# Performance work log

Hardware: AMD Instinct MI355X
Metric: run time of the kernel (lower is better)

## Reference

```python
import jax, jax.numpy as jnp
import numpy as np

B, S, D, H, E, K = 2, 2048, 1024, 16, 8, 2
HD = D // H          # head dim = 64 (single shared KV head: MQA)
HID = 4 * D          # MoE expert hidden dim


def _rmsnorm(x):
    # zeta SimpleRMSNorm: F.normalize(x, dim=-1) * dim**0.5
    n = jnp.linalg.norm(x, axis=-1, keepdims=True)
    return x / jnp.maximum(n, 1e-12) * (D ** 0.5)


def setup_inputs() -> dict:
    key = jax.random.key(0)
    ks = jax.random.split(key, 8)
    def w(k, shape, fan_in):
        return jax.random.normal(k, shape, jnp.float32) * (fan_in ** -0.5)
    return {
        "x":  jax.random.normal(ks[0], (B, S, D), jnp.float32),
        "Wq": w(ks[1], (D, D), D),
        "Wk": w(ks[2], (D, HD), D),
        "Wv": w(ks[3], (D, HD), D),
        "Wo": w(ks[4], (D, D), D),
        "Wg": w(ks[5], (D, E), D),
        "W1": w(ks[6], (E, D, HID), D),
        "W2": w(ks[7], (E, HID, D), HID),
    }


def reference(x, Wq, Wk, Wv, Wo, Wg, W1, W2):
    skip = x
    # --- pre-norm + multi-query attention + residual ---
    h = _rmsnorm(x)
    q = (h @ Wq).reshape(B, S, H, HD)           # [B,S,H,HD]
    k = h @ Wk                                   # [B,S,HD] shared kv head
    v = h @ Wv                                   # [B,S,HD]
    scores = jnp.einsum('bqhd,bkd->bhqk', q, k) * (HD ** -0.5)
    attn = jax.nn.softmax(scores, axis=-1)
    o = jnp.einsum('bhqk,bkd->bqhd', attn, v).reshape(B, S, D) @ Wo
    x = o + h
    # --- pre-norm + MoE (top-k softmax gating over experts) ---
    h2 = _rmsnorm(x)
    logits = h2 @ Wg                             # [B,S,E]
    topv, topi = jax.lax.top_k(logits, K)        # [B,S,K]
    gate = jax.nn.softmax(topv, axis=-1)         # renormalized top-k weights
    # dense combine weights [B,S,E], zero for unselected experts
    dense_w = jnp.sum(jax.nn.one_hot(topi, E, dtype=h2.dtype) * gate[..., None], axis=-2)
    moe_out = jnp.zeros_like(h2)
    for e in range(E):  # fixed small expert count
        ffn = jax.nn.gelu(h2 @ W1[e]) @ W2[e]
        moe_out = moe_out + dense_w[..., e:e + 1] * ffn
    return moe_out + skip
```

## Files before the change

kernel.cpp:

```cpp
#include <hip/hip_runtime.h>

typedef __bf16 bf16x8 __attribute__((ext_vector_type(8)));
typedef float f32x4 __attribute__((ext_vector_type(4)));
using u16 = unsigned short;
using u32 = unsigned int;

#define B_   2
#define S_   2048
#define D_   1024
#define E_   8
#define HID_ 4096
#define M_   4096

__device__ __forceinline__ u16 f2b_rne(float f) {
    unsigned u = __float_as_uint(f);
    u += 0x7fffu + ((u >> 16) & 1u);
    return (u16)(u >> 16);
}
__device__ __forceinline__ float b2f(u16 h) { return __uint_as_float(((unsigned)h) << 16); }
__device__ __forceinline__ void split2(float v, u16& h, u16& m) {
    h = f2b_rne(v); m = f2b_rne(v - b2f(h));
}
__device__ __forceinline__ void gld16(void* l, const void* g) {
    __builtin_amdgcn_global_load_lds((const __attribute__((address_space(1))) u32*)g,
                                     (__attribute__((address_space(3))) u32*)l, 16, 0, 0);
}

static constexpr size_t OFF_WQKVT0 = 0;
static constexpr size_t OFF_WQKVT1 = OFF_WQKVT0 + (size_t)1152*1024*2;
static constexpr size_t OFF_WOT    = OFF_WQKVT1 + (size_t)1152*1024*2;
static constexpr size_t OFF_W1T    = OFF_WOT    + (size_t)1024*1024*2;
static constexpr size_t OFF_W2T    = OFF_W1T    + (size_t)E_*HID_*D_*2;
static constexpr size_t OFF_WOWG   = OFF_W2T    + (size_t)E_*HID_*D_*2;
static constexpr size_t OFF_HF32   = OFF_WOWG   + (size_t)1024*8*4;
static constexpr size_t OFF_H0     = OFF_HF32   + (size_t)M_*D_*4;
static constexpr size_t OFF_H1     = OFF_H0     + (size_t)M_*D_*2;
static constexpr size_t OFF_H2     = OFF_H1     + (size_t)M_*D_*2;
static constexpr size_t OFF_CTL    = OFF_H2     + (size_t)M_*D_*2;
static constexpr size_t OFF_TEXP   = OFF_CTL    + 512;
static constexpr size_t OFF_TGATE  = OFF_TEXP   + (size_t)M_*2*4;
static constexpr size_t OFF_R2T    = OFF_TGATE  + (size_t)M_*2*4;
static constexpr size_t OFF_T2R    = OFF_R2T    + (size_t)9216*4;
static constexpr size_t OFF_ZROW   = OFF_T2R    + (size_t)M_*2*4;
static constexpr size_t OFF_BIG    = OFF_ZROW   + 4096;
static constexpr size_t OFF_Q0     = OFF_BIG;
static constexpr size_t OFF_Q1     = OFF_Q0   + (size_t)M_*D_*2;
static constexpr size_t OFF_KF0    = OFF_Q1   + (size_t)M_*D_*2;
static constexpr size_t OFF_KF1    = OFF_KF0  + (size_t)2*128*2*512*2;
static constexpr size_t OFF_VF0    = OFF_KF1  + (size_t)2*128*2*512*2;
static constexpr size_t OFF_VF1    = OFF_VF0  + (size_t)2*64*4*512*2;
static constexpr size_t OFF_OF32   = OFF_VF1  + (size_t)2*64*4*512*2;
static constexpr size_t OFF_AOBF   = OFF_OF32 + (size_t)M_*D_*4;
static constexpr size_t OFF_XF32   = OFF_Q0;
static constexpr size_t OFF_TACT   = OFF_BIG;
static constexpr size_t OFF_CONTR  = OFF_TACT + (size_t)9216*HID_*2;

__global__ __launch_bounds__(256) void transpose_split2_k(const float* __restrict__ in,
        u16* __restrict__ o0, u16* __restrict__ o1, int R, int C)
{
    __shared__ float tile[32][33];
    int tx = threadIdx.x & 31, ty = threadIdx.x >> 5;
    int c0 = blockIdx.x * 32, r0 = blockIdx.y * 32;
#pragma unroll
    for (int k = 0; k < 4; ++k)
        tile[ty + k*8][tx] = in[(size_t)(r0 + ty + k*8)*C + c0 + tx];
    __syncthreads();
#pragma unroll
    for (int k = 0; k < 4; ++k) {
        float v = tile[tx][ty + k*8];
        u16 h, m; split2(v, h, m);
        size_t idx = (size_t)(c0 + ty + k*8)*R + r0 + tx;
        o0[idx] = h; o1[idx] = m;
    }
}

__global__ __launch_bounds__(256) void transpose_k(const float* __restrict__ in,
                                                   u16* __restrict__ out, int R, int C)
{
    __shared__ u16 tile[32][33];
    int bz = blockIdx.z;
    in  += (size_t)bz * R * C;
    out += (size_t)bz * R * C;
    int tx = threadIdx.x & 31, ty = threadIdx.x >> 5;
    int c0 = blockIdx.x * 32, r0 = blockIdx.y * 32;
#pragma unroll
    for (int k = 0; k < 4; ++k)
        tile[ty + k*8][tx] = f2b_rne(in[(size_t)(r0 + ty + k*8)*C + c0 + tx]);
    __syncthreads();
#pragma unroll
    for (int k = 0; k < 4; ++k)
        out[(size_t)(c0 + ty + k*8)*R + r0 + tx] = tile[tx][ty + k*8];
}

__global__ __launch_bounds__(64) void wowg_k(const float* __restrict__ Wo,
                                             const float* __restrict__ Wg,
                                             float* __restrict__ wowg)
{
    int i = blockIdx.x, lane = threadIdx.x;
    const float* wr = Wo + (size_t)i*1024;
    float acc[8] = {};
#pragma unroll
    for (int j = 0; j < 16; ++j) {
        int d = j*64 + lane;
        float wv = wr[d];
        const float* g = Wg + (size_t)d*8;
        float4 g0 = *(const float4*)g, g1 = *(const float4*)(g + 4);
        acc[0] += wv*g0.x; acc[1] += wv*g0.y; acc[2] += wv*g0.z; acc[3] += wv*g0.w;
        acc[4] += wv*g1.x; acc[5] += wv*g1.y; acc[6] += wv*g1.z; acc[7] += wv*g1.w;
    }
#pragma unroll
    for (int e = 0; e < 8; ++e)
#pragma unroll
        for (int o = 32; o; o >>= 1) acc[e] += __shfl_down(acc[e], o);
    if (lane == 0) {
#pragma unroll
        for (int e = 0; e < 8; ++e) wowg[i*8 + e] = acc[e];
    }
}

__global__ __launch_bounds__(256) void rmsnorm1_k(const float* __restrict__ x,
                                                  float* __restrict__ hf,
                                                  u16* __restrict__ h0, u16* __restrict__ h1)
{
    int row = blockIdx.x, t = threadIdx.x;
    float4 v = ((const float4*)(x + (size_t)row*1024))[t];
    float ss = v.x*v.x + v.y*v.y + v.z*v.z + v.w*v.w;
#pragma unroll
    for (int o = 32; o; o >>= 1) ss += __shfl_down(ss, o);
    __shared__ float red[4];
    if ((t & 63) == 0) red[t >> 6] = ss;
    __syncthreads();
    float tot = red[0] + red[1] + red[2] + red[3];
    float sc = 32.0f / fmaxf(sqrtf(tot), 1e-12f);
    float vv[4] = {v.x*sc, v.y*sc, v.z*sc, v.w*sc};
    ((float4*)(hf + (size_t)row*1024))[t] = *(float4*)vv;
    u16 a0[4], a1[4];
#pragma unroll
    for (int j = 0; j < 4; ++j) split2(vv[j], a0[j], a1[j]);
    *(uint2*)(h0 + (size_t)row*1024 + t*4) = *(uint2*)a0;
    *(uint2*)(h1 + (size_t)row*1024 + t*4) = *(uint2*)a1;
}

__device__ __forceinline__ void gemm_pass(const u16* __restrict__ gA0, const u16* __restrict__ gB0,
                                          u16* As, u16* Bs, f32x4 (&acc)[4][4],
                                          int t, const int (&aoff)[4], const int (&boff)[4])
{
    const u16* gA1 = gA0 + (size_t)64*1024;
    const u16* gB1 = gB0 + (size_t)64*1024;
    uint4 ra0 = *(const uint4*)gA0, ra1 = *(const uint4*)gA1;
    uint4 rb0 = *(const uint4*)gB0, rb1 = *(const uint4*)gB1;
    for (int kt = 0; kt < 32; ++kt) {
        __syncthreads();
        *(uint4*)((char*)As + t*16)        = ra0;
        *(uint4*)((char*)As + 4096 + t*16) = ra1;
        *(uint4*)((char*)Bs + t*16)        = rb0;
        *(uint4*)((char*)Bs + 4096 + t*16) = rb1;
        __syncthreads();
        if (kt + 1 < 32) {
            int k0 = (kt + 1)*32;
            ra0 = *(const uint4*)(gA0 + k0); ra1 = *(const uint4*)(gA1 + k0);
            rb0 = *(const uint4*)(gB0 + k0); rb1 = *(const uint4*)(gB1 + k0);
        }
        bf16x8 av[4], bv[4];
#pragma unroll
        for (int i = 0; i < 4; ++i) av[i] = *(const bf16x8*)((char*)As + aoff[i]);
#pragma unroll
        for (int i = 0; i < 4; ++i) bv[i] = *(const bf16x8*)((char*)Bs + boff[i]);
#pragma unroll
        for (int mi = 0; mi < 4; ++mi)
#pragma unroll
            for (int ni = 0; ni < 4; ++ni)
                acc[mi][ni] = __builtin_amdgcn_mfma_f32_16x16x32_bf16(av[mi], bv[ni], acc[mi][ni], 0, 0, 0);
    }
}

__global__ __launch_bounds__(256) void gemm_qkv(
    const u16* __restrict__ A0, const u16* __restrict__ A1,
    const u16* __restrict__ B0, const u16* __restrict__ B1,
    u16* __restrict__ q0, u16* __restrict__ q1,
    u16* __restrict__ kf0, u16* __restrict__ kf1,
    u16* __restrict__ vf0, u16* __restrict__ vf1)
{
    int rb = blockIdx.x, cb = blockIdx.y;
    __shared__ __attribute__((aligned(16))) u16 As[4096];
    __shared__ __attribute__((aligned(16))) u16 Bs[4096];
    int t = threadIdx.x, w = t >> 6, lane = t & 63, r = lane & 15, g = lane >> 4;
    int wr = w >> 1, wc = w & 1;
    int arow0 = t >> 2, colA = (t & 3)*8;
    int aoff[4], boff[4];
#pragma unroll
    for (int i = 0; i < 4; ++i) {
        aoff[i] = ((wr*64 + i*16 + r)*32 + g*8)*2;
        boff[i] = ((wc*64 + i*16 + r)*32 + g*8)*2;
    }
    f32x4 acc[4][4] = {};
    const u16* Aps[3]; const u16* Bps[3];
    Aps[0] = A0; Aps[1] = A0; Aps[2] = A1;
    Bps[0] = B0; Bps[1] = B1; Bps[2] = B0;
#pragma unroll
    for (int c = 0; c < 3; ++c) {
        const u16* Ab = Aps[c] + (size_t)(rb*128 + arow0)*1024 + colA;
        const u16* Bb = Bps[c] + (size_t)(cb*128 + arow0)*1024 + colA;
        gemm_pass(Ab, Bb, As, Bs, acc, t, aoff, boff);
    }
    int bm = rb*128, bn = cb*128;
#pragma unroll
    for (int mi = 0; mi < 4; ++mi)
#pragma unroll
        for (int ni = 0; ni < 4; ++ni) {
            int row0 = bm + wr*64 + mi*16 + g*4;
            int col  = bn + wc*64 + ni*16 + r;
#pragma unroll
            for (int reg = 0; reg < 4; ++reg) {
                float val = acc[mi][ni][reg];
                int rr = row0 + reg;
                if (col < 1024) {
                    u16 hh, mm; split2(val * 0.125f, hh, mm);
                    size_t idx = (size_t)rr*1024 + col;
                    q0[idx] = hh; q1[idx] = mm;
                } else {
                    int c = col - 1024;
                    u16 hh, mm; split2(val, hh, mm);
                    int bb = rr >> 11, kv = rr & 2047;
                    if (c < 64) {
                        int ntg = kv >> 4, r2 = kv & 15, kc = c >> 5, gg = (c >> 3) & 3, j = c & 7;
                        size_t off = ((((size_t)bb*128 + ntg)*2 + kc)*64 + gg*16 + r2)*8 + j;
                        kf0[off] = hh; kf1[off] = mm;
                    } else {
                        int d = c - 64;
                        int ntg = d >> 4, r2 = d & 15, kvc = kv >> 5, gg = (kv >> 3) & 3, j = kv & 7;
                        size_t off = ((((size_t)bb*64 + kvc)*4 + ntg)*64 + gg*16 + r2)*8 + j;
                        vf0[off] = hh; vf1[off] = mm;
                    }
                }
            }
        }
}

__global__ __launch_bounds__(256) void attn_k(
    const u16* __restrict__ q0, const u16* __restrict__ q1,
    const u16* __restrict__ kfr0, const u16* __restrict__ kfr1,
    const u16* __restrict__ vfr0, const u16* __restrict__ vfr1,
    float* __restrict__ of32, u16* __restrict__ obf)
{
    int qt = blockIdx.x, h = blockIdx.y, b = blockIdx.z;
    int t = threadIdx.x, w = t >> 6, lane = t & 63, r = lane & 15, g = lane >> 4;
    __shared__ __attribute__((aligned(16))) char smem[40960];
    char* plw = smem + 32768 + w*2048;

    const char* K0c = (const char*)kfr0;
    const char* K1c = (const char*)kfr1;
    const char* V0c = (const char*)vfr0;
    const char* V1c = (const char*)vfr1;

    int qrow = b*2048 + qt*64 + w*16 + r;
    bf16x8 qf0[2], qf1[2];
#pragma unroll
    for (int kc = 0; kc < 2; ++kc) {
        size_t qi = (size_t)qrow*1024 + h*64 + kc*32 + g*8;
        qf0[kc] = *(const bf16x8*)(q0 + qi);
        qf1[kc] = *(const bf16x8*)(q1 + qi);
    }

    f32x4 accO[4] = {};
    float mrun[4], lrun[4];
#pragma unroll
    for (int reg = 0; reg < 4; ++reg) { mrun[reg] = -1e30f; lrun[reg] = 0.f; }

    for (int kt = 0; kt < 32; ++kt) {
        __syncthreads();
        {
            size_t kb = ((size_t)(b*128 + kt*4))*2048;
            gld16(smem +         t*16, K0c + kb + t*16);
            gld16(smem + 4096  + t*16, K0c + kb + 4096 + t*16);
            gld16(smem + 8192  + t*16, K1c + kb + t*16);
            gld16(smem + 12288 + t*16, K1c + kb + 4096 + t*16);
            size_t vb = ((size_t)(b*64 + kt*2))*4096;
            gld16(smem + 16384 + t*16, V0c + vb + t*16);
            gld16(smem + 20480 + t*16, V0c + vb + 4096 + t*16);
            gld16(smem + 24576 + t*16, V1c + vb + t*16);
            gld16(smem + 28672 + t*16, V1c + vb + 4096 + t*16);
        }
        __syncthreads();

        f32x4 s[4] = {};
#pragma unroll
        for (int nt = 0; nt < 4; ++nt)
#pragma unroll
            for (int kc = 0; kc < 2; ++kc) {
                bf16x8 kf0 = *(const bf16x8*)(smem + (nt*2 + kc)*1024 + lane*16);
                bf16x8 kf1 = *(const bf16x8*)(smem + 8192 + (nt*2 + kc)*1024 + lane*16);
                s[nt] = __builtin_amdgcn_mfma_f32_16x16x32_bf16(qf0[kc], kf0, s[nt], 0, 0, 0);
                s[nt] = __builtin_amdgcn_mfma_f32_16x16x32_bf16(qf0[kc], kf1, s[nt], 0, 0, 0);
                s[nt] = __builtin_amdgcn_mfma_f32_16x16x32_bf16(qf1[kc], kf0, s[nt], 0, 0, 0);
            }

#pragma unroll
        for (int reg = 0; reg < 4; ++reg) {
            float mx = fmaxf(fmaxf(s[0][reg], s[1][reg]), fmaxf(s[2][reg], s[3][reg]));
#pragma unroll
            for (int d = 1; d < 16; d <<= 1) mx = fmaxf(mx, __shfl_xor(mx, d));
            float mn = fmaxf(mrun[reg], mx);
            float alpha = __expf(mrun[reg] - mn);
            float ls = 0.f;
#pragma unroll
            for (int nt = 0; nt < 4; ++nt) {
                float pv = __expf(s[nt][reg] - mn);
                s[nt][reg] = pv; ls += pv;
            }
#pragma unroll
            for (int d = 1; d < 16; d <<= 1) ls += __shfl_xor(ls, d);
            lrun[reg] = lrun[reg]*alpha + ls;
            mrun[reg] = mn;
#pragma unroll
            for (int nt = 0; nt < 4; ++nt) accO[nt][reg] *= alpha;
        }

#pragma unroll
        for (int ps = 0; ps < 2; ++ps) {
#pragma unroll
            for (int nt = 0; nt < 4; ++nt)
#pragma unroll
                for (int reg = 0; reg < 4; ++reg) {
                    float pv = s[nt][reg];
                    u16 hh = f2b_rne(pv);
                    if (ps) hh = f2b_rne(pv - b2f(hh));
                    int gr = g*4 + reg;
                    int off = (gr*128 + (nt*16 + r)*2) ^ ((gr & 7) << 4);
                    *(u16*)(plw + off) = hh;
                }
#pragma unroll
            for (int kc = 0; kc < 2; ++kc) {
                int po = (r*128 + kc*64 + g*16) ^ ((r & 7) << 4);
                bf16x8 pf = *(const bf16x8*)(plw + po);
#pragma unroll
                for (int nt = 0; nt < 4; ++nt) {
                    bf16x8 vf0 = *(const bf16x8*)(smem + 16384 + (kc*4 + nt)*1024 + lane*16);
                    accO[nt] = __builtin_amdgcn_mfma_f32_16x16x32_bf16(pf, vf0, accO[nt], 0, 0, 0);
                    if (ps == 0) {
                        bf16x8 vf1 = *(const bf16x8*)(smem + 24576 + (kc*4 + nt)*1024 + lane*16);
                        accO[nt] = __builtin_amdgcn_mfma_f32_16x16x32_bf16(pf, vf1, accO[nt], 0, 0, 0);
                    }
                }
            }
        }
    }

#pragma unroll
    for (int nt = 0; nt < 4; ++nt)
#pragma unroll
        for (int reg = 0; reg < 4; ++reg) {
            float o = accO[nt][reg] / lrun[reg];
            int row = b*2048 + qt*64 + w*16 + g*4 + reg;
            size_t idx = (size_t)row*1024 + h*64 + nt*16 + r;
            of32[idx] = o;
            obf[idx] = f2b_rne(o);
        }
}

template<int EP, bool MOE, bool INDIR>
__global__ __launch_bounds__(256) void gemm1(
    const u16* __restrict__ Abase, const u16* __restrict__ Bbase,
    u16* __restrict__ outb, float* __restrict__ outf, const float* __restrict__ addsrc,
    const int* __restrict__ r2t, const int* __restrict__ ctl, const u16* __restrict__ zrow,
    int K, int N)
{
    int rb = blockIdx.x, cb = blockIdx.y;
    if (MOE) { if (rb*128 >= ctl[16]) return; }
    const u16* Bt = Bbase;
    if (MOE) Bt += (size_t)ctl[32 + rb] * N * K;

    __shared__ __attribute__((aligned(16))) u16 As[4096];
    __shared__ __attribute__((aligned(16))) u16 Bs[4096];
    int t = threadIdx.x, w = t >> 6, lane = t & 63, r = lane & 15, g = lane >> 4;
    int wr = w >> 1, wc = w & 1;
    int arow0 = t >> 2, colA = (t & 3)*8;

    const char *gA0c, *gA1c;
    if (INDIR) {
        int tk0 = r2t[rb*128 + arow0];
        int tk1 = r2t[rb*128 + 64 + arow0];
        gA0c = (const char*)((tk0 < 0 ? zrow : Abase + (size_t)tk0*K) + colA);
        gA1c = (const char*)((tk1 < 0 ? zrow : Abase + (size_t)tk1*K) + colA);
    } else {
        gA0c = (const char*)(Abase + (size_t)(rb*128 + arow0)*K + colA);
        gA1c = (const char*)(Abase + (size_t)(rb*128 + 64 + arow0)*K + colA);
    }
    const char* gB0c = (const char*)(Bt + (size_t)(cb*128 + arow0)*K + colA);
    const char* gB1c = (const char*)(Bt + (size_t)(cb*128 + 64 + arow0)*K + colA);

    int aoff[4], boff[4];
#pragma unroll
    for (int i = 0; i < 4; ++i) {
        aoff[i] = ((wr*64 + i*16 + r)*32 + g*8)*2;
        boff[i] = ((wc*64 + i*16 + r)*32 + g*8)*2;
    }
    f32x4 acc[4][4] = {};
    int nk = K >> 5;
    for (int kt = 0; kt < nk; ++kt) {
        __syncthreads();
        gld16((char*)As + t*16,        gA0c + kt*64);
        gld16((char*)As + 4096 + t*16, gA1c + kt*64);
        gld16((char*)Bs + t*16,        gB0c + kt*64);
        gld16((char*)Bs + 4096 + t*16, gB1c + kt*64);
        __syncthreads();
        bf16x8 av[4], bv[4];
#pragma unroll
        for (int i = 0; i < 4; ++i) av[i] = *(const bf16x8*)((char*)As + aoff[i]);
#pragma unroll
        for (int i = 0; i < 4; ++i) bv[i] = *(const bf16x8*)((char*)Bs + boff[i]);
#pragma unroll
        for (int mi = 0; mi < 4; ++mi)
#pragma unroll
            for (int ni = 0; ni < 4; ++ni)
                acc[mi][ni] = __builtin_amdgcn_mfma_f32_16x16x32_bf16(av[mi], bv[ni], acc[mi][ni], 0, 0, 0);
    }

    int bm = rb*128, bn = cb*128;
#pragma unroll
    for (int mi = 0; mi < 4; ++mi)
#pragma unroll
        for (int ni = 0; ni < 4; ++ni) {
            int row0 = bm + wr*64 + mi*16 + g*4;
            int col  = bn + wc*64 + ni*16 + r;
#pragma unroll
            for (int reg = 0; reg < 4; ++reg) {
                float val = acc[mi][ni][reg];
                int rr = row0 + reg;
                size_t idx = (size_t)rr*N + col;
                if (EP == 0) {
                    outf[idx] = val + addsrc[idx];
                } else if (EP == 1) {
                    float u  = 1.5957691216f * (val + 0.044715f*val*val*val);
                    outb[idx] = f2b_rne(val / (1.0f + __expf(-u)));
                } else {
                    outb[idx] = f2b_rne(val);
                }
            }
        }
}

__global__ __launch_bounds__(64) void gate_k(const float* __restrict__ x2,
                                             const float* __restrict__ hrow,
                                             const float* __restrict__ orow,
                                             const float* __restrict__ Wg,
                                             const float* __restrict__ wowg,
                                             u16* __restrict__ h2,
                                             int* __restrict__ texp, float* __restrict__ tgate,
                                             int* __restrict__ ctl)
{
    int tkn = blockIdx.x, lane = threadIdx.x;
    const float* xr = x2   + (size_t)tkn*1024;
    const float* hr = hrow + (size_t)tkn*1024;
    const float* orp = orow + (size_t)tkn*1024;
    float xv[16];
    float ss = 0.f;
    float acc[8] = {};
#pragma unroll
    for (int j = 0; j < 16; ++j) {
        int d = j*64 + lane;
        float xf = xr[d]; xv[j] = xf; ss += xf*xf;
        float hf = hr[d], of = orp[d];
        const float* wg = Wg + (size_t)d*8;
        const float* wo = wowg + (size_t)d*8;
        float4 a0 = *(const float4*)wg, a1 = *(const float4*)(wg + 4);
        float4 b0 = *(const float4*)wo, b1 = *(const float4*)(wo + 4);
        acc[0] += hf*a0.x + of*b0.x; acc[1] += hf*a0.y + of*b0.y;
        acc[2] += hf*a0.z + of*b0.z; acc[3] += hf*a0.w + of*b0.w;
        acc[4] += hf*a1.x + of*b1.x; acc[5] += hf*a1.y + of*b1.y;
        acc[6] += hf*a1.z + of*b1.z; acc[7] += hf*a1.w + of*b1.w;
    }
#pragma unroll
    for (int o = 32; o; o >>= 1) ss += __shfl_down(ss, o);
    ss = __shfl(ss, 0);
    float sc = 32.0f / fmaxf(sqrtf(ss), 1e-12f);
#pragma unroll
    for (int j = 0; j < 16; ++j)
        h2[(size_t)tkn*1024 + j*64 + lane] = f2b_rne(xv[j]*sc);
#pragma unroll
    for (int e = 0; e < 8; ++e)
#pragma unroll
        for (int o = 32; o; o >>= 1) acc[e] += __shfl_down(acc[e], o);
    if (lane == 0) {
        float lg[8];
#pragma unroll
        for (int e = 0; e < 8; ++e) lg[e] = acc[e]*sc;
        int i0 = 0; float v0 = lg[0];
#pragma unroll
        for (int e = 1; e < 8; ++e) if (lg[e] > v0) { v0 = lg[e]; i0 = e; }
        int i1 = -1; float v1 = -1e30f;
#pragma unroll
        for (int e = 0; e < 8; ++e) if (e != i0 && lg[e] > v1) { v1 = lg[e]; i1 = e; }
        float g0 = 1.0f / (1.0f + __expf(v1 - v0));
        texp[tkn*2] = i0; texp[tkn*2+1] = i1;
        tgate[tkn*2] = g0; tgate[tkn*2+1] = 1.0f - g0;
        atomicAdd(&ctl[i0], 1); atomicAdd(&ctl[i1], 1);
    }
}

__global__ void plan_k(int* ctl, int* r2t)
{
    if (threadIdx.x == 0) {
        int off = 0;
        for (int e = 0; e < 8; ++e) {
            int c = ctl[e];
            ctl[8 + e] = off;
            int p = (c + 127) & ~127;
            int rb0 = off >> 7, nrbe = p >> 7;
            for (int i = 0; i < nrbe; ++i) ctl[32 + rb0 + i] = e;
            off += p;
        }
        ctl[16] = off; ctl[17] = off >> 7;
    }
    __syncthreads();
    for (int i = threadIdx.x; i < 9216; i += blockDim.x) r2t[i] = -1;
}

__global__ __launch_bounds__(256) void assign_k(const int* __restrict__ texp, int* ctl,
                                                int* __restrict__ r2t, int* __restrict__ t2r)
{
    int tkn = blockIdx.x*256 + threadIdx.x;
    if (tkn >= M_) return;
#pragma unroll
    for (int kk = 0; kk < 2; ++kk) {
        int e = texp[tkn*2 + kk];
        int pos = atomicAdd(&ctl[8 + e], 1);
        r2t[pos] = tkn;
        t2r[tkn*2 + kk] = pos;
    }
}

__global__ __launch_bounds__(256) void combine_k(const float* __restrict__ xin,
                                                 const u16* __restrict__ contrib,
                                                 const int* __restrict__ t2r,
                                                 const float* __restrict__ tgate,
                                                 float* __restrict__ out)
{
    int tkn = blockIdx.x;
    int c = threadIdx.x*4;
    int r0 = t2r[tkn*2], r1 = t2r[tkn*2+1];
    float g0 = tgate[tkn*2], g1 = tgate[tkn*2+1];
    float4 sk = *(const float4*)(xin + (size_t)tkn*1024 + c);
    const u16* c0p = contrib + (size_t)r0*1024 + c;
    const u16* c1p = contrib + (size_t)r1*1024 + c;
    float4 o;
    o.x = sk.x + g0*b2f(c0p[0]) + g1*b2f(c1p[0]);
    o.y = sk.y + g0*b2f(c0p[1]) + g1*b2f(c1p[1]);
    o.z = sk.z + g0*b2f(c0p[2]) + g1*b2f(c1p[2]);
    o.w = sk.w + g0*b2f(c0p[3]) + g1*b2f(c1p[3]);
    *(float4*)(out + (size_t)tkn*1024 + c) = o;
}

extern "C" void kernel_launch(void* const* d_in, const int* in_sizes, int n_in,
                              void* d_out, int out_size, void* d_ws, size_t ws_size,
                              hipStream_t stream)
{
    const float* x  = (const float*)d_in[0];
    const float* Wq = (const float*)d_in[1];
    const float* Wk = (const float*)d_in[2];
    const float* Wv = (const float*)d_in[3];
    const float* Wo = (const float*)d_in[4];
    const float* Wg = (const float*)d_in[5];
    const float* W1 = (const float*)d_in[6];
    const float* W2 = (const float*)d_in[7];
    float* out = (float*)d_out;

    char* ws = (char*)d_ws;
    auto U = [&](size_t off) { return (u16*)(ws + off); };
    auto F = [&](size_t off) { return (float*)(ws + off); };
    int*   CTL  = (int*)(ws + OFF_CTL);
    int*   TEXP = (int*)(ws + OFF_TEXP);
    float* TGATE= (float*)(ws + OFF_TGATE);
    int*   R2T  = (int*)(ws + OFF_R2T);
    int*   T2R  = (int*)(ws + OFF_T2R);

    hipMemsetAsync(ws + OFF_CTL,  0, 512,  stream);
    hipMemsetAsync(ws + OFF_ZROW, 0, 4096, stream);

    dim3 tb(256);
    transpose_split2_k<<<dim3(32, 32), tb, 0, stream>>>(Wq, U(OFF_WQKVT0), U(OFF_WQKVT1), 1024, 1024);
    transpose_split2_k<<<dim3(2, 32),  tb, 0, stream>>>(Wk, U(OFF_WQKVT0) + (size_t)1024*1024, U(OFF_WQKVT1) + (size_t)1024*1024, 1024, 64);
    transpose_split2_k<<<dim3(2, 32),  tb, 0, stream>>>(Wv, U(OFF_WQKVT0) + (size_t)1088*1024, U(OFF_WQKVT1) + (size_t)1088*1024, 1024, 64);
    transpose_k<<<dim3(32, 32, 1), tb, 0, stream>>>(Wo, U(OFF_WOT), 1024, 1024);
    transpose_k<<<dim3(128, 32, 8), tb, 0, stream>>>(W1, U(OFF_W1T), 1024, 4096);
    transpose_k<<<dim3(32, 128, 8), tb, 0, stream>>>(W2, U(OFF_W2T), 4096, 1024);
    wowg_k<<<1024, 64, 0, stream>>>(Wo, Wg, F(OFF_WOWG));

    rmsnorm1_k<<<M_, 256, 0, stream>>>(x, F(OFF_HF32), U(OFF_H0), U(OFF_H1));

    gemm_qkv<<<dim3(32, 9), tb, 0, stream>>>(U(OFF_H0), U(OFF_H1),
        U(OFF_WQKVT0), U(OFF_WQKVT1),
        U(OFF_Q0), U(OFF_Q1), U(OFF_KF0), U(OFF_KF1), U(OFF_VF0), U(OFF_VF1));

    attn_k<<<dim3(32, 16, 2), tb, 0, stream>>>(U(OFF_Q0), U(OFF_Q1),
        U(OFF_KF0), U(OFF_KF1), U(OFF_VF0), U(OFF_VF1), F(OFF_OF32), U(OFF_AOBF));

    gemm1<0, false, false><<<dim3(32, 8), tb, 0, stream>>>(U(OFF_AOBF), U(OFF_WOT),
        nullptr, F(OFF_XF32), F(OFF_HF32), nullptr, nullptr, nullptr, 1024, 1024);

    gate_k<<<M_, 64, 0, stream>>>(F(OFF_XF32), F(OFF_HF32), F(OFF_OF32), Wg, F(OFF_WOWG),
        U(OFF_H2), TEXP, TGATE, CTL);
    plan_k<<<1, 256, 0, stream>>>(CTL, R2T);
    assign_k<<<16, 256, 0, stream>>>(TEXP, CTL, R2T, T2R);

    gemm1<1, true, true ><<<dim3(72, 32), tb, 0, stream>>>(U(OFF_H2), U(OFF_W1T),
        U(OFF_TACT), nullptr, nullptr, R2T, CTL, U(OFF_ZROW), 1024, 4096);
    gemm1<2, true, false><<<dim3(72, 8),  tb, 0, stream>>>(U(OFF_TACT), U(OFF_W2T),
        U(OFF_CONTR), nullptr, nullptr, nullptr, CTL, nullptr, 4096, 1024);

    combine_k<<<M_, 256, 0, stream>>>(x, U(OFF_CONTR), T2R, TGATE, out);
}
```

Measured before the change: 1.057 ms.

## Retile QKV GEMM, widen attention blocks, add 64-row MoE down GEMM, batch gate

The QKV GEMM now uses 64-row tiles and fuses the three split-precision passes into one K loop, loading tiles with direct global-to-LDS copies so each A/B tile is fetched once. The attention kernel runs 512 threads per block covering 128 queries, sharing each K/V tile load across twice as many waves. A dedicated 64-row-tile kernel for the second MoE GEMM replaces the generic one, giving more blocks. The gate kernel processes four tokens per 256-thread block. These raise parallelism and cut redundant loads, but the GEMMs lose the register prefetch of the next tile, which risks exposing load latency.

```diff
diff --git a/kernel.cpp b/kernel.cpp
--- a/kernel.cpp
+++ b/kernel.cpp
@@ -141,39 +141,6 @@
     *(uint2*)(h1 + (size_t)row*1024 + t*4) = *(uint2*)a1;
 }
 
-__device__ __forceinline__ void gemm_pass(const u16* __restrict__ gA0, const u16* __restrict__ gB0,
-                                          u16* As, u16* Bs, f32x4 (&acc)[4][4],
-                                          int t, const int (&aoff)[4], const int (&boff)[4])
-{
-    const u16* gA1 = gA0 + (size_t)64*1024;
-    const u16* gB1 = gB0 + (size_t)64*1024;
-    uint4 ra0 = *(const uint4*)gA0, ra1 = *(const uint4*)gA1;
-    uint4 rb0 = *(const uint4*)gB0, rb1 = *(const uint4*)gB1;
-    for (int kt = 0; kt < 32; ++kt) {
-        __syncthreads();
-        *(uint4*)((char*)As + t*16)        = ra0;
-        *(uint4*)((char*)As + 4096 + t*16) = ra1;
-        *(uint4*)((char*)Bs + t*16)        = rb0;
-        *(uint4*)((char*)Bs + 4096 + t*16) = rb1;
-        __syncthreads();
-        if (kt + 1 < 32) {
-            int k0 = (kt + 1)*32;
-            ra0 = *(const uint4*)(gA0 + k0); ra1 = *(const uint4*)(gA1 + k0);
-            rb0 = *(const uint4*)(gB0 + k0); rb1 = *(const uint4*)(gB1 + k0);
-        }
-        bf16x8 av[4], bv[4];
-#pragma unroll
-        for (int i = 0; i < 4; ++i) av[i] = *(const bf16x8*)((char*)As + aoff[i]);
-#pragma unroll
-        for (int i = 0; i < 4; ++i) bv[i] = *(const bf16x8*)((char*)Bs + boff[i]);
-#pragma unroll
-        for (int mi = 0; mi < 4; ++mi)
-#pragma unroll
-            for (int ni = 0; ni < 4; ++ni)
-                acc[mi][ni] = __builtin_amdgcn_mfma_f32_16x16x32_bf16(av[mi], bv[ni], acc[mi][ni], 0, 0, 0);
-    }
-}
-
 __global__ __launch_bounds__(256) void gemm_qkv(
     const u16* __restrict__ A0, const u16* __restrict__ A1,
     const u16* __restrict__ B0, const u16* __restrict__ B1,
@@ -182,34 +149,54 @@
     u16* __restrict__ vf0, u16* __restrict__ vf1)
 {
     int rb = blockIdx.x, cb = blockIdx.y;
-    __shared__ __attribute__((aligned(16))) u16 As[4096];
-    __shared__ __attribute__((aligned(16))) u16 Bs[4096];
+    __shared__ __attribute__((aligned(16))) char L[24576];
     int t = threadIdx.x, w = t >> 6, lane = t & 63, r = lane & 15, g = lane >> 4;
     int wr = w >> 1, wc = w & 1;
-    int arow0 = t >> 2, colA = (t & 3)*8;
-    int aoff[4], boff[4];
-#pragma unroll
-    for (int i = 0; i < 4; ++i) {
-        aoff[i] = ((wr*64 + i*16 + r)*32 + g*8)*2;
-        boff[i] = ((wc*64 + i*16 + r)*32 + g*8)*2;
-    }
-    f32x4 acc[4][4] = {};
-    const u16* Aps[3]; const u16* Bps[3];
-    Aps[0] = A0; Aps[1] = A0; Aps[2] = A1;
-    Bps[0] = B0; Bps[1] = B1; Bps[2] = B0;
-#pragma unroll
-    for (int c = 0; c < 3; ++c) {
-        const u16* Ab = Aps[c] + (size_t)(rb*128 + arow0)*1024 + colA;
-        const u16* Bb = Bps[c] + (size_t)(cb*128 + arow0)*1024 + colA;
-        gemm_pass(Ab, Bb, As, Bs, acc, t, aoff, boff);
-    }
-    int bm = rb*128, bn = cb*128;
-#pragma unroll
-    for (int mi = 0; mi < 4; ++mi)
+    int arow = t >> 2, colA = (t & 3)*8;
+
+    const char* a0c = (const char*)(A0 + (size_t)(rb*64  + arow)*1024 + colA);
+    const char* a1c = (const char*)(A1 + (size_t)(rb*64  + arow)*1024 + colA);
+    const char* b0c = (const char*)(B0 + (size_t)(cb*128 + arow)*1024 + colA);
+    const char* b1c = (const char*)(B1 + (size_t)(cb*128 + arow)*1024 + colA);
+    const size_t BH = (size_t)64*1024*2;
+
+    int aoff[2], boff[4];
+#pragma unroll
+    for (int i = 0; i < 2; ++i) aoff[i] = ((wr*32 + i*16 + r)*32 + g*8)*2;
+#pragma unroll
+    for (int i = 0; i < 4; ++i) boff[i] = ((wc*64 + i*16 + r)*32 + g*8)*2;
+
+    f32x4 acc[2][4] = {};
+    for (int kt = 0; kt < 32; ++kt) {
+        __syncthreads();
+        gld16(L +          t*16, a0c + kt*64);
+        gld16(L + 4096  +  t*16, a1c + kt*64);
+        gld16(L + 8192  +  t*16, b0c + kt*64);
+        gld16(L + 12288 +  t*16, b0c + BH + kt*64);
+        gld16(L + 16384 +  t*16, b1c + kt*64);
+        gld16(L + 20480 +  t*16, b1c + BH + kt*64);
+        __syncthreads();
+        bf16x8 a0v[2], a1v[2], b0v[4], b1v[4];
+#pragma unroll
+        for (int i = 0; i < 2; ++i) { a0v[i] = *(const bf16x8*)(L + aoff[i]); a1v[i] = *(const bf16x8*)(L + 4096 + aoff[i]); }
+#pragma unroll
+        for (int i = 0; i < 4; ++i) { b0v[i] = *(const bf16x8*)(L + 8192 + boff[i]); b1v[i] = *(const bf16x8*)(L + 16384 + boff[i]); }
+#pragma unroll
+        for (int mi = 0; mi < 2; ++mi)
+#pragma unroll
+            for (int ni = 0; ni < 4; ++ni) {
+                acc[mi][ni] = __builtin_amdgcn_mfma_f32_16x16x32_bf16(a0v[mi], b0v[ni], acc[mi][ni], 0, 0, 0);
+                acc[mi][ni] = __builtin_amdgcn_mfma_f32_16x16x32_bf16(a0v[mi], b1v[ni], acc[mi][ni], 0, 0, 0);
+                acc[mi][ni] = __builtin_amdgcn_mfma_f32_16x16x32_bf16(a1v[mi], b0v[ni], acc[mi][ni], 0, 0, 0);
+            }
+    }
+
+#pragma unroll
+    for (int mi = 0; mi < 2; ++mi)
 #pragma unroll
         for (int ni = 0; ni < 4; ++ni) {
-            int row0 = bm + wr*64 + mi*16 + g*4;
-            int col  = bn + wc*64 + ni*16 + r;
+            int row0 = rb*64 + wr*32 + mi*16 + g*4;
+            int col  = cb*128 + wc*64 + ni*16 + r;
 #pragma unroll
             for (int reg = 0; reg < 4; ++reg) {
                 float val = acc[mi][ni][reg];
@@ -237,7 +224,7 @@
         }
 }
 
-__global__ __launch_bounds__(256) void attn_k(
+__global__ __launch_bounds__(512) void attn_k(
     const u16* __restrict__ q0, const u16* __restrict__ q1,
     const u16* __restrict__ kfr0, const u16* __restrict__ kfr1,
     const u16* __restrict__ vfr0, const u16* __restrict__ vfr1,
@@ -245,7 +232,7 @@
 {
     int qt = blockIdx.x, h = blockIdx.y, b = blockIdx.z;
     int t = threadIdx.x, w = t >> 6, lane = t & 63, r = lane & 15, g = lane >> 4;
-    __shared__ __attribute__((aligned(16))) char smem[40960];
+    __shared__ __attribute__((aligned(16))) char smem[49152];
     char* plw = smem + 32768 + w*2048;
 
     const char* K0c = (const char*)kfr0;
@@ -253,7 +240,7 @@
     const char* V0c = (const char*)vfr0;
     const char* V1c = (const char*)vfr1;
 
-    int qrow = b*2048 + qt*64 + w*16 + r;
+    int qrow = b*2048 + qt*128 + w*16 + r;
     bf16x8 qf0[2], qf1[2];
 #pragma unroll
     for (int kc = 0; kc < 2; ++kc) {
@@ -271,15 +258,11 @@
         __syncthreads();
         {
             size_t kb = ((size_t)(b*128 + kt*4))*2048;
-            gld16(smem +         t*16, K0c + kb + t*16);
-            gld16(smem + 4096  + t*16, K0c + kb + 4096 + t*16);
-            gld16(smem + 8192  + t*16, K1c + kb + t*16);
-            gld16(smem + 12288 + t*16, K1c + kb + 4096 + t*16);
-            size_t vb = ((size_t)(b*64 + kt*2))*4096;
-            gld16(smem + 16384 + t*16, V0c + vb + t*16);
-            gld16(smem + 20480 + t*16, V0c + vb + 4096 + t*16);
-            gld16(smem + 24576 + t*16, V1c + vb + t*16);
-            gld16(smem + 28672 + t*16, V1c + vb + 4096 + t*16);
+            size_t vb = ((size_t)(b*64  + kt*2))*4096;
+            gld16(smem +          t*16, K0c + kb + t*16);
+            gld16(smem + 8192  +  t*16, K1c + kb + t*16);
+            gld16(smem + 16384 +  t*16, V0c + vb + t*16);
+            gld16(smem + 24576 +  t*16, V1c + vb + t*16);
         }
         __syncthreads();
 
@@ -351,7 +334,7 @@
 #pragma unroll
         for (int reg = 0; reg < 4; ++reg) {
             float o = accO[nt][reg] / lrun[reg];
-            int row = b*2048 + qt*64 + w*16 + g*4 + reg;
+            int row = b*2048 + qt*128 + w*16 + g*4 + reg;
             size_t idx = (size_t)row*1024 + h*64 + nt*16 + r;
             of32[idx] = o;
             obf[idx] = f2b_rne(o);
@@ -440,7 +423,61 @@
         }
 }
 
-__global__ __launch_bounds__(64) void gate_k(const float* __restrict__ x2,
+__global__ __launch_bounds__(256) void gemm_moe2(
+    const u16* __restrict__ Abase, const u16* __restrict__ Bbase,
+    u16* __restrict__ outb, const int* __restrict__ ctl)
+{
+    int rb = blockIdx.x, cb = blockIdx.y;
+    if (rb*64 >= ctl[16]) return;
+    const u16* Bt = Bbase + (size_t)ctl[32 + (rb >> 1)] * (size_t)1024 * 4096;
+
+    __shared__ __attribute__((aligned(16))) char L[12288];
+    int t = threadIdx.x, w = t >> 6, lane = t & 63, r = lane & 15, g = lane >> 4;
+    int wr = w >> 1, wc = w & 1;
+    int arow = t >> 2, colA = (t & 3)*8;
+
+    const char* aC = (const char*)(Abase + (size_t)(rb*64  + arow)*4096 + colA);
+    const char* bC = (const char*)(Bt    + (size_t)(cb*128 + arow)*4096 + colA);
+    const size_t BH = (size_t)64*4096*2;
+
+    int aoff[2], boff[4];
+#pragma unroll
+    for (int i = 0; i < 2; ++i) aoff[i] = ((wr*32 + i*16 + r)*32 + g*8)*2;
+#pragma unroll
+    for (int i = 0; i < 4; ++i) boff[i] = ((wc*64 + i*16 + r)*32 + g*8)*2;
+
+    f32x4 acc[2][4] = {};
+    for (int kt = 0; kt < 128; ++kt) {
+        __syncthreads();
+        gld16(L +         t*16, aC + kt*64);
+        gld16(L + 4096 +  t*16, bC + kt*64);
+        gld16(L + 8192 +  t*16, bC + BH + kt*64);
+        __syncthreads();
+        bf16x8 av[2], bv[4];
+#pragma unroll
+        for (int i = 0; i < 2; ++i) av[i] = *(const bf16x8*)(L + aoff[i]);
+#pragma unroll
+        for (int i = 0; i < 4; ++i) bv[i] = *(const bf16x8*)(L + 4096 + boff[i]);
+#pragma unroll
+        for (int mi = 0; mi < 2; ++mi)
+#pragma unroll
+            for (int ni = 0; ni < 4; ++ni)
+                acc[mi][ni] = __builtin_amdgcn_mfma_f32_16x16x32_bf16(av[mi], bv[ni], acc[mi][ni], 0, 0, 0);
+    }
+
+#pragma unroll
+    for (int mi = 0; mi < 2; ++mi)
+#pragma unroll
+        for (int ni = 0; ni < 4; ++ni) {
+            int row0 = rb*64 + wr*32 + mi*16 + g*4;
+            int col  = cb*128 + wc*64 + ni*16 + r;
+#pragma unroll
+            for (int reg = 0; reg < 4; ++reg)
+                outb[(size_t)(row0 + reg)*1024 + col] = f2b_rne(acc[mi][ni][reg]);
+        }
+}
+
+__global__ __launch_bounds__(256) void gate_k(const float* __restrict__ x2,
                                              const float* __restrict__ hrow,
                                              const float* __restrict__ orow,
                                              const float* __restrict__ Wg,
@@ -449,9 +486,10 @@
                                              int* __restrict__ texp, float* __restrict__ tgate,
                                              int* __restrict__ ctl)
 {
-    int tkn = blockIdx.x, lane = threadIdx.x;
-    const float* xr = x2   + (size_t)tkn*1024;
-    const float* hr = hrow + (size_t)tkn*1024;
+    int tkn = blockIdx.x*4 + (threadIdx.x >> 6);
+    int lane = threadIdx.x & 63;
+    const float* xr  = x2   + (size_t)tkn*1024;
+    const float* hr  = hrow + (size_t)tkn*1024;
     const float* orp = orow + (size_t)tkn*1024;
     float xv[16];
     float ss = 0.f;
@@ -588,25 +626,24 @@
 
     rmsnorm1_k<<<M_, 256, 0, stream>>>(x, F(OFF_HF32), U(OFF_H0), U(OFF_H1));
 
-    gemm_qkv<<<dim3(32, 9), tb, 0, stream>>>(U(OFF_H0), U(OFF_H1),
+    gemm_qkv<<<dim3(64, 9), tb, 0, stream>>>(U(OFF_H0), U(OFF_H1),
         U(OFF_WQKVT0), U(OFF_WQKVT1),
         U(OFF_Q0), U(OFF_Q1), U(OFF_KF0), U(OFF_KF1), U(OFF_VF0), U(OFF_VF1));
 
-    attn_k<<<dim3(32, 16, 2), tb, 0, stream>>>(U(OFF_Q0), U(OFF_Q1),
+    attn_k<<<dim3(16, 16, 2), dim3(512), 0, stream>>>(U(OFF_Q0), U(OFF_Q1),
         U(OFF_KF0), U(OFF_KF1), U(OFF_VF0), U(OFF_VF1), F(OFF_OF32), U(OFF_AOBF));
 
     gemm1<0, false, false><<<dim3(32, 8), tb, 0, stream>>>(U(OFF_AOBF), U(OFF_WOT),
         nullptr, F(OFF_XF32), F(OFF_HF32), nullptr, nullptr, nullptr, 1024, 1024);
 
-    gate_k<<<M_, 64, 0, stream>>>(F(OFF_XF32), F(OFF_HF32), F(OFF_OF32), Wg, F(OFF_WOWG),
+    gate_k<<<1024, 256, 0, stream>>>(F(OFF_XF32), F(OFF_HF32), F(OFF_OF32), Wg, F(OFF_WOWG),
         U(OFF_H2), TEXP, TGATE, CTL);
     plan_k<<<1, 256, 0, stream>>>(CTL, R2T);
     assign_k<<<16, 256, 0, stream>>>(TEXP, CTL, R2T, T2R);
 
     gemm1<1, true, true ><<<dim3(72, 32), tb, 0, stream>>>(U(OFF_H2), U(OFF_W1T),
         U(OFF_TACT), nullptr, nullptr, R2T, CTL, U(OFF_ZROW), 1024, 4096);
-    gemm1<2, true, false><<<dim3(72, 8),  tb, 0, stream>>>(U(OFF_TACT), U(OFF_W2T),
-        U(OFF_CONTR), nullptr, nullptr, nullptr, CTL, nullptr, 4096, 1024);
+    gemm_moe2<<<dim3(144, 8), tb, 0, stream>>>(U(OFF_TACT), U(OFF_W2T), U(OFF_CONTR), CTL);
 
     combine_k<<<M_, 256, 0, stream>>>(x, U(OFF_CONTR), T2R, TGATE, out);
 }
```

Result: slower. 1.080 ms (+2.2%).
